# Performance work log

Measured on AMD Instinct MI355X. Metric: run time of the kernel, lower is better.

## Reference

```python
import itertools
import jax, jax.numpy as jnp
import numpy as np

FFT_LEN = 256      # kernel_size['ae']
HOP = 64           # frame hop
N_ANCHOR = 6
N_SPK = 2
NUM_STACKS = 4
N_DIL = 8          # dilations 1,2,...,128
EMBED = 20
OUTPUT_RATIO = 0.5
EPS = 1e-12        # tf.contrib.layers.layer_norm epsilon
DILS = [2 ** i for i in range(N_DIL)]
COMBS = np.array(list(itertools.combinations(range(N_ANCHOR), N_SPK)), np.int32)  # [15,2]
# sqrt of periodic hann window (scipy.signal.hann(256, sym=False))
WIN = np.sqrt(0.5 - 0.5 * np.cos(2.0 * np.pi * np.arange(FFT_LEN) / FFT_LEN)).astype(np.float32)
_wsq = WIN ** 2
_denom = np.tile(_wsq.reshape(FFT_LEN // HOP, HOP).sum(0), FFT_LEN // HOP)
INV_WIN = (WIN / _denom).astype(np.float32)  # tf.signal.inverse_stft_window_fn


def _prelu(x, a):
    return jnp.maximum(x, 0) + a * jnp.minimum(x, 0)


def _cln(x, g, b):  # layer norm over channel axis only (begin_norm_axis=2)
    m = x.mean(-1, keepdims=True)
    v = ((x - m) ** 2).mean(-1, keepdims=True)
    return (x - m) / jnp.sqrt(v + EPS) * g + b


def _gln(x, g, b):  # global layer norm over (time, channel) (begin_norm_axis=1)
    m = x.mean((1, 2), keepdims=True)
    v = ((x - m) ** 2).mean((1, 2), keepdims=True)
    return (x - m) / jnp.sqrt(v + EPS) * g + b


def _dwconv(x, w, di):  # x:[B,T,C], w:[K,C]; dilated depthwise conv, SAME padding
    C = x.shape[-1]
    return jax.lax.conv_general_dilated(
        x, w[:, None, :], (1,), 'SAME', rhs_dilation=(di,),
        dimension_numbers=('NWC', 'WIO', 'NWC'), feature_group_count=C)


def _ola(frames, hop):  # overlap-and-add: [.., T, K] -> [.., (T-1)*hop + K]
    lead = frames.shape[:-2]
    T, K = frames.shape[-2:]
    L = (T - 1) * hop + K
    idx = (np.arange(T)[:, None] * hop + np.arange(K)).reshape(-1)
    return jnp.zeros(lead + (L,), frames.dtype).at[..., idx].add(frames.reshape(lead + (T * K,)))


def _forward(audios, enc_w, enc_b, bottle_gamma, bottle_beta, bottle_w, bottle_b,
             blk_c1_w, blk_c1_b, blk_p1, blk_g1_g, blk_g1_b, blk_dw,
             blk_p2, blk_g2_g, blk_g2_b, blk_c2_w, blk_c2_b,
             sep_w, sep_b, anchors, dec_w, dec_b):
    B, _, L = audios.shape
    mix = audios.sum(1)                                   # [B,L]
    T = (L - FFT_LEN) // HOP + 1                          # 497 frames
    idx = np.arange(T)[:, None] * HOP + np.arange(FFT_LEN)
    frames = mix[:, idx]                                  # [B,T,256]
    enc = jax.nn.relu(jnp.einsum('btk,kf->btf', frames, enc_w) + enc_b)  # learned encoder
    spec = jnp.fft.rfft(frames * WIN)                     # STFT [B,T,129]
    mag = jnp.abs(spec)
    phase = jnp.arctan2(spec.imag, spec.real)
    x = _cln(jnp.concatenate([enc, jnp.log1p(mag)], -1), bottle_gamma, bottle_beta)
    x = x @ bottle_w + bottle_b                           # bottleneck 1x1 conv -> [B,T,256]
    for i in range(NUM_STACKS * N_DIL):                   # TCN dilated blocks
        di = DILS[i % N_DIL]
        y = x @ blk_c1_w[i] + blk_c1_b[i]
        y = _gln(_prelu(y, blk_p1[i]), blk_g1_g[i], blk_g1_b[i])
        y = _dwconv(y, blk_dw[i], di)
        y = _gln(_prelu(y, blk_p2[i]), blk_g2_g[i], blk_g2_b[i])
        x = x + (y @ blk_c2_w[i] + blk_c2_b[i])
    Fc = enc.shape[-1] + mag.shape[-1]                    # 385 = concat_channels
    emb = (x @ sep_w + sep_b).reshape(B, T, Fc, EMBED)    # [B,T,F,E]
    a_sets = anchors[COMBS]                               # [15,2,E]
    assign = jax.nn.softmax(jnp.einsum('btfe,pce->bptfc', emb, a_sets), axis=-1)
    attr = jnp.einsum('bptfc,btfe->bpce', assign, emb) / assign.sum((2, 3))[..., None]
    sp = jnp.einsum('bpce,bpde->bpcd', attr, attr)        # pairwise attractor similarity
    sp = jnp.where(jnp.eye(N_SPK, dtype=bool), -jnp.inf, sp)
    choice = jnp.argmin(sp.max((-1, -2)), axis=1)         # most dissimilar subset
    attractors = attr[jnp.arange(B), choice]              # [B,C,E]
    logits = jnp.einsum('btfe,bce->bctf', emb, attractors)
    feat = jnp.concatenate([enc, mag], -1)                # [B,T,F]
    code = logits * feat[:, None]                         # [B,C,T,F]
    ae_f = enc.shape[-1]
    conv_out = _ola(code[..., :ae_f] @ dec_w + dec_b, HOP)  # learned decoder branch
    ph = phase[:, None]
    sm = code[..., ae_f:]                                 # last stft_ch channels
    istft_frames = jnp.fft.irfft(jax.lax.complex(jnp.cos(ph) * sm, jnp.sin(ph) * sm), n=FFT_LEN)
    istft = _ola(istft_frames * INV_WIN, HOP)             # iSTFT branch
    return conv_out * OUTPUT_RATIO + istft * (1.0 - OUTPUT_RATIO)


def setup_inputs():
    B, S, L = 8, 2, 32000
    AE, BTL, H, K = 256, 256, 512, 3
    NB = NUM_STACKS * N_DIL
    FC = AE + FFT_LEN // 2 + 1
    ks = jax.random.split(jax.random.key(0), 9)
    rn = lambda k, sh, s=0.05: jax.random.normal(k, sh, jnp.float32) * s
    return {
        'audios': jax.random.normal(ks[0], (B, S, L), jnp.float32),
        'enc_w': rn(ks[1], (FFT_LEN, AE)),
        'enc_b': jnp.zeros((AE,), jnp.float32),
        'bottle_gamma': jnp.ones((FC,), jnp.float32),
        'bottle_beta': jnp.zeros((FC,), jnp.float32),
        'bottle_w': rn(ks[2], (FC, BTL)),
        'bottle_b': jnp.zeros((BTL,), jnp.float32),
        'blk_c1_w': rn(ks[3], (NB, BTL, H)),
        'blk_c1_b': jnp.zeros((NB, H), jnp.float32),
        'blk_p1': jnp.zeros((NB, H), jnp.float32),
        'blk_g1_g': jnp.ones((NB, H), jnp.float32),
        'blk_g1_b': jnp.zeros((NB, H), jnp.float32),
        'blk_dw': rn(ks[4], (NB, K, H), 0.2),
        'blk_p2': jnp.zeros((NB, H), jnp.float32),
        'blk_g2_g': jnp.ones((NB, H), jnp.float32),
        'blk_g2_b': jnp.zeros((NB, H), jnp.float32),
        'blk_c2_w': rn(ks[5], (NB, H, BTL)),
        'blk_c2_b': jnp.zeros((NB, BTL), jnp.float32),
        'sep_w': rn(ks[6], (BTL, FC * EMBED), 0.02),
        'sep_b': jnp.zeros((FC * EMBED,), jnp.float32),
        'anchors': rn(ks[7], (N_ANCHOR, EMBED), 0.1),
        'dec_w': rn(ks[8], (AE, FFT_LEN)),
        'dec_b': jnp.zeros((FFT_LEN,), jnp.float32),
    }


def reference(audios, enc_w, enc_b, bottle_gamma, bottle_beta, bottle_w, bottle_b,
              blk_c1_w, blk_c1_b, blk_p1, blk_g1_g, blk_g1_b, blk_dw,
              blk_p2, blk_g2_g, blk_g2_b, blk_c2_w, blk_c2_b,
              sep_w, sep_b, anchors, dec_w, dec_b):
    return _forward(audios, enc_w, enc_b, bottle_gamma, bottle_beta, bottle_w, bottle_b,
                    blk_c1_w, blk_c1_b, blk_p1, blk_g1_g, blk_g1_b, blk_dw,
                    blk_p2, blk_g2_g, blk_g2_b, blk_c2_w, blk_c2_b,
                    sep_w, sep_b, anchors, dec_w, dec_b)
```

## Files before the change

kernel.cpp:

```cpp
#include <hip/hip_runtime.h>
#include <math.h>

#define B_ 8
#define S_ 2
#define L_ 32000
#define T_ 497
#define AE 256
#define NFREQ 129
#define FC 385
#define XSTR 388
#define FRSTR 516
#define AFSTR 516
#define BTL 256
#define H_ 512
#define NB 32
#define EMBED 20
#define KB (T_*FC)
#define MEPS 1e-12f
#define PI2F 6.28318530717958647692f
#define MTOT (B_*T_)
#define SEPN 7700
#define SEPNT16 484
#define SEPBLK 7623

typedef __attribute__((ext_vector_type(8))) short bf16x8;
typedef __attribute__((ext_vector_type(4))) float f32x4;

__device__ __forceinline__ ushort f2bf(float f){
  union { float f; unsigned u; } x; x.f = f;
  unsigned r = x.u + 0x7FFFu + ((x.u >> 16) & 1u);
  return (ushort)(r >> 16);
}
__device__ __forceinline__ float bf2f(ushort h){
  union { unsigned u; float f; } x; x.u = ((unsigned)h) << 16;
  return x.f;
}

__device__ __forceinline__ float aldf(const float* p){
  return __hip_atomic_load(p, __ATOMIC_RELAXED, __HIP_MEMORY_SCOPE_AGENT);
}

static constexpr size_t ALGN(size_t x){ return (x + 63) & ~(size_t)63; }
static constexpr size_t o_bfr  = 0;
static constexpr size_t o_decB = ALGN(o_bfr + (size_t)256*516);
static constexpr size_t o_decBias = ALGN(o_decB + (size_t)514*256);
static constexpr size_t o_biasF  = ALGN(o_decBias + 256);
static constexpr size_t o_cf   = ALGN(o_biasF + 516);
static constexpr size_t o_mag  = ALGN(o_cf + (size_t)B_*T_*FRSTR);
static constexpr size_t o_cosp = ALGN(o_mag + (size_t)B_*T_*NFREQ);
static constexpr size_t o_sinp = ALGN(o_cosp + (size_t)B_*T_*NFREQ);
static constexpr size_t o_xln  = ALGN(o_sinp + (size_t)B_*T_*NFREQ);
static constexpr size_t o_x    = ALGN(o_xln + (size_t)B_*T_*XSTR);
static constexpr size_t o_y    = ALGN(o_x + (size_t)B_*T_*BTL);
static constexpr size_t o_z    = ALGN(o_y + (size_t)B_*T_*H_);
static constexpr size_t o_gsum = ALGN(o_z + (size_t)B_*T_*H_);
static constexpr size_t o_acc  = o_gsum + 1024;
static constexpr size_t o_att  = ALGN(o_acc + (size_t)B_*16*21);
static constexpr size_t o_emb  = ALGN(o_att + (size_t)B_*2*EMBED);
static constexpr size_t o_Af   = ALGN(o_emb + (size_t)B_*KB*EMBED);
static constexpr size_t o_w1p  = ALGN(o_Af + (size_t)2*B_*T_*AFSTR);
static constexpr size_t o_w2p  = ALGN(o_w1p + (size_t)2097152);
static constexpr size_t o_c1c2 = ALGN(o_w2p + (size_t)2097152);
static constexpr size_t o_bar  = ALGN(o_c1c2 + (size_t)32*512);
static constexpr size_t o_fr   = o_y;

#define PREP_BLOCKS 1034
#define PACKW_BLOCKS 32768
#define BIAS2_BLOCKS 256
#define PACKSEP_BLOCKS 7744

__global__ __launch_bounds__(256) void k_setup(
    const float* __restrict__ enc_w, const float* __restrict__ enc_b,
    const float* __restrict__ dec_w, const float* __restrict__ dec_b,
    const float* __restrict__ c1_w, const float* __restrict__ c2_w,
    const float* __restrict__ g2_g, const float* __restrict__ g2_b,
    const float* __restrict__ sep_w,
    float* __restrict__ bfr, float* __restrict__ decB,
    float* __restrict__ decBias, float* __restrict__ biasF,
    ushort* __restrict__ w1p, ushort* __restrict__ w2p,
    float* __restrict__ c1c2, ushort* __restrict__ w3p)
{
  int bx = blockIdx.x;
  if (bx < PREP_BLOCKS){
    int i = bx*256 + threadIdx.x;
    if (i < 256*516){
      int k = i / 516, n = i % 516;
      float v;
      if (n < 256) v = enc_w[(size_t)k*256 + n];
      else if (n < 514){
        int f2 = n - 256;
        float win = sqrtf(0.5f - 0.5f*cosf(PI2F * (float)k / 256.0f));
        int f = (f2 < NFREQ) ? f2 : (f2 - NFREQ);
        int m = (k * f) & 255;
        float th = PI2F * (float)m / 256.0f;
        v = (f2 < NFREQ) ? win * cosf(th) : -win * sinf(th);
      } else v = 0.f;
      bfr[i] = v;
      return;
    }
    int j = i - 256*516;
    if (j < 514*256){
      int k = j / 256, n = j & 255;
      float v;
      if (k < 256){
        v = 0.5f * dec_w[(size_t)k*256 + n];
      } else {
        int m = n & 63;
        float den = 0.f;
        #pragma unroll
        for (int q = 0; q < 4; q++) den += 0.5f - 0.5f*cosf(PI2F*(float)(m + 64*q)/256.0f);
        float win = sqrtf(0.5f - 0.5f*cosf(PI2F*(float)n/256.0f));
        float iw = win / den;
        int f = (k < 385) ? (k - 256) : (k - 385);
        int mm = (f * n) & 255;
        float th = PI2F * (float)mm / 256.0f;
        if (k < 385){
          float cf = (f==0 || f==128) ? 1.0f : 2.0f;
          v = 0.5f * iw * cf * cosf(th) * (1.0f/256.0f);
        } else {
          v = (f==0 || f==128) ? 0.0f : -1.0f * iw * sinf(th) * (1.0f/256.0f);
        }
      }
      decB[j] = v;
      return;
    }
    int jj = j - 514*256;
    if (jj < 256){ decBias[jj] = 0.5f * dec_b[jj]; return; }
    int n = jj - 256;
    if (n < 516) biasF[n] = (n < 256) ? enc_b[n] : 0.f;
    return;
  }
  if (bx < PREP_BLOCKS + PACKW_BLOCKS){
    size_t idx = (size_t)(bx - PREP_BLOCKS)*256 + threadIdx.x;
    const size_t PER = (size_t)32*131072;
    if (idx < PER){
      int i = (int)(idx >> 17);
      int o = (int)(idx & 131071);
      int kc = o >> 14;
      int n16 = (o >> 9) & 31;
      int l = (o >> 3) & 63;
      int j = o & 7;
      int k = kc*32 + (l>>4)*8 + j;
      int n = n16*16 + (l&15);
      w1p[idx] = f2bf(c1_w[((size_t)i*256 + k)*512 + n]);
    } else {
      size_t o2 = idx - PER;
      int i = (int)(o2 >> 17);
      int o = (int)(o2 & 131071);
      int kc = o >> 13;
      int n16 = (o >> 9) & 15;
      int l = (o >> 3) & 63;
      int j = o & 7;
      int k = kc*32 + (l>>4)*8 + j;
      int n = n16*16 + (l&15);
      w2p[o2] = f2bf(g2_g[(size_t)i*512 + k] * c2_w[((size_t)i*512 + k)*256 + n]);
    }
    return;
  }
  if (bx < PREP_BLOCKS + PACKW_BLOCKS + BIAS2_BLOCKS){
    int bi = bx - (PREP_BLOCKS + PACKW_BLOCKS);
    int i = bi >> 3, ks = bi & 7;
    int n = threadIdx.x;
    float s1 = 0.f, s2 = 0.f;
    for (int k = ks*64; k < ks*64 + 64; k++){
      float w = c2_w[((size_t)i*512 + k)*256 + n];
      s1 = fmaf(g2_b[(size_t)i*512 + k], w, s1);
      s2 = fmaf(g2_g[(size_t)i*512 + k], w, s2);
    }
    atomicAdd(&c1c2[(size_t)i*512 + n], s1);
    atomicAdd(&c1c2[(size_t)i*512 + 256 + n], s2);
    return;
  }
  {
    size_t idx = (size_t)(bx - (PREP_BLOCKS + PACKW_BLOCKS + BIAS2_BLOCKS))*256 + threadIdx.x;
    int j = (int)(idx & 7);
    int l = (int)((idx >> 3) & 63);
    int rest = (int)(idx >> 9);
    int n16 = rest % SEPNT16;
    int kc = rest / SEPNT16;
    int k = kc*32 + (l>>4)*8 + j;
    int n = n16*16 + (l&15);
    w3p[idx] = (n < SEPN) ? f2bf(sep_w[(size_t)k*SEPN + n]) : (ushort)0;
  }
}

template<int ALOAD>
__global__ __launch_bounds__(256, 2) void gemm3(
    const float* __restrict__ A, const float* __restrict__ Bm,
    const float* __restrict__ bias, float* __restrict__ C,
    int M, int N, int K, int lda, int ldb, int relu_cols)
{
  __shared__ float As[16][68];
  __shared__ float Bs[16][68];
  const int tid = threadIdx.x;
  const int tx = tid & 15, ty = tid >> 4;
  const int row0 = blockIdx.y*64, col0 = blockIdx.x*64;
  const int am = tid >> 2, ak = (tid & 3)*4;
  const int bk = tid >> 4, bn = (tid & 15)*4;
  const int arow = row0 + am;
  const bool aok = arow < M;
  const float* aptr = nullptr;
  const float* ap0 = nullptr; const float* ap1 = nullptr;
  if (ALOAD == 2){
    int r = aok ? arow : 0;
    int b = r / T_, t = r % T_;
    ap0 = A + ((size_t)b*2)*L_ + t*64;
    ap1 = ap0 + L_;
  } else {
    aptr = A + (size_t)(aok ? arow : 0)*lda;
  }
  const bool bfull = (col0 + 64 <= N);
  const int ksteps = (K+15) >> 4;

  float4 av, bv;

#define LOADA(ks_) { int k0 = (ks_) << 4; \
    av = make_float4(0.f,0.f,0.f,0.f); \
    if (aok){ \
      if (ALOAD == 2){ \
        float4 u = *(const float4*)(ap0 + k0 + ak); \
        float4 w = *(const float4*)(ap1 + k0 + ak); \
        av.x = u.x+w.x; av.y = u.y+w.y; av.z = u.z+w.z; av.w = u.w+w.w; \
      } else if (k0 + ak + 4 <= lda){ \
        av = *(const float4*)(aptr + k0 + ak); \
      } else { \
        float* pv = (float*)&av; \
        for (int j = 0; j < 4; j++){ int k = k0+ak+j; if (k < K) pv[j] = aptr[k]; } \
      } \
    } }

#define LOADB(ks_) { int k = ((ks_) << 4) + bk; \
    bv = make_float4(0.f,0.f,0.f,0.f); \
    if (k < K){ \
      if (bfull) bv = *(const float4*)(Bm + (size_t)k*ldb + col0 + bn); \
      else { float* pv = (float*)&bv; \
        for (int j = 0; j < 4; j++){ int c = col0+bn+j; if (c < N) pv[j] = Bm[(size_t)k*ldb + c]; } } } }

  float acc[4][4] = {};
  LOADA(0); LOADB(0);
  for (int ks = 0; ks < ksteps; ks++){
    As[ak+0][am] = av.x; As[ak+1][am] = av.y;
    As[ak+2][am] = av.z; As[ak+3][am] = av.w;
    *(float4*)&Bs[bk][bn] = bv;
    __syncthreads();
    if (ks + 1 < ksteps){ LOADA(ks+1); LOADB(ks+1); }
    #pragma unroll
    for (int kk = 0; kk < 16; kk++){
      float a4[4], b4[4];
      *(float4*)a4 = *(const float4*)&As[kk][ty*4];
      *(float4*)b4 = *(const float4*)&Bs[kk][tx*4];
      #pragma unroll
      for (int i = 0; i < 4; i++)
        #pragma unroll
        for (int j = 0; j < 4; j++) acc[i][j] = fmaf(a4[i], b4[j], acc[i][j]);
    }
    __syncthreads();
  }
#undef LOADA
#undef LOADB

  float bb4[4];
  #pragma unroll
  for (int j = 0; j < 4; j++){
    int c = col0 + tx*4 + j;
    bb4[j] = (bias && c < N) ? bias[c] : 0.f;
  }
  #pragma unroll
  for (int i = 0; i < 4; i++){
    int r_l = row0 + ty*4 + i;
    if (r_l >= M) continue;
    size_t r_g = (size_t)r_l;
    int c0 = col0 + tx*4;
    if (bfull){
      float4 o; float* po = (float*)&o;
      #pragma unroll
      for (int j = 0; j < 4; j++){
        float v = acc[i][j] + bb4[j];
        if (c0 + j < relu_cols) v = fmaxf(v, 0.f);
        po[j] = v;
      }
      *(float4*)(C + r_g*N + c0) = o;
    } else {
      #pragma unroll
      for (int j = 0; j < 4; j++){
        int c = c0 + j;
        if (c >= N) continue;
        float v = acc[i][j] + bb4[j];
        if (c < relu_cols) v = fmaxf(v, 0.f);
        C[r_g*N + c] = v;
      }
    }
  }
}

__global__ __launch_bounds__(256, 2) void k_sep(
    const ushort* __restrict__ xb, const ushort* __restrict__ wp,
    const float* __restrict__ bias, float* __restrict__ C)
{
  int id = blockIdx.x;
  int xcd = id & 7, sub = id >> 3;
  const int q = SEPBLK/8, r = SEPBLK%8;
  int lin = (xcd < r ? xcd*(q+1) : r*(q+1) + (xcd - r)*q) + sub;
  int nb = lin/63, mt = lin%63;
  int tid = threadIdx.x;
  int wv = tid >> 6, l = tid & 63;
  int row0 = mt*64 + wv*16;
  int lm = l & 15, lq = l >> 4;
  int row = row0 + lm;
  int rclamp = (row < MTOT) ? row : (MTOT-1);
  int n0 = nb*64;
  const ushort* ap = xb + (size_t)rclamp*256;
  f32x4 acc[4] = {};
  #pragma unroll
  for (int kc = 0; kc < 8; kc++){
    bf16x8 a = *(const bf16x8*)(ap + kc*32 + lq*8);
    #pragma unroll
    for (int nt = 0; nt < 4; nt++){
      bf16x8 bfv = *(const bf16x8*)(wp + (((size_t)kc*SEPNT16 + (n0>>4) + nt)*64 + l)*8);
      acc[nt] = __builtin_amdgcn_mfma_f32_16x16x32_bf16(a, bfv, acc[nt], 0, 0, 0);
    }
  }
  #pragma unroll
  for (int nt = 0; nt < 4; nt++){
    int col = n0 + nt*16 + lm;
    if (col >= SEPN) continue;
    float bb = bias[col];
    #pragma unroll
    for (int r2 = 0; r2 < 4; r2++){
      int t = row0 + lq*4 + r2;
      if (t < MTOT) C[(size_t)t*SEPN + col] = acc[nt][r2] + bb;
    }
  }
}

__device__ __forceinline__ void pbar(unsigned* bar, int grp){
  __syncthreads();
  if (threadIdx.x == 0){
    unsigned* g = bar + grp*64;
    unsigned gen = __hip_atomic_load(g+32, __ATOMIC_RELAXED, __HIP_MEMORY_SCOPE_AGENT);
    unsigned p = gen & 1u;
    unsigned a = __hip_atomic_fetch_add(g+p, 1u, __ATOMIC_RELAXED, __HIP_MEMORY_SCOPE_AGENT);
    if (a == 63u){
      __hip_atomic_store(g+p, 0u, __ATOMIC_RELAXED, __HIP_MEMORY_SCOPE_AGENT);
      __hip_atomic_store(g+32, gen+1u, __ATOMIC_RELAXED, __HIP_MEMORY_SCOPE_AGENT);
    } else {
      while (__hip_atomic_load(g+32, __ATOMIC_RELAXED, __HIP_MEMORY_SCOPE_AGENT) == gen)
        __builtin_amdgcn_s_sleep(1);
    }
    asm volatile("buffer_inv sc0" ::: "memory");
  }
  __syncthreads();
}

__global__ __launch_bounds__(256, 2) void k_tcn(
    float* __restrict__ x0, float* __restrict__ x1,
    float* __restrict__ Ubuf, ushort* __restrict__ yb,
    const ushort* __restrict__ w1pA, const ushort* __restrict__ w2pA,
    const float* __restrict__ c1bA, const float* __restrict__ p1A,
    const float* __restrict__ g1gA, const float* __restrict__ g1bA,
    const float* __restrict__ dwA, const float* __restrict__ p2A,
    const float* __restrict__ c2bA, const float* __restrict__ ccA,
    float* __restrict__ gsum, unsigned* bar)
{
  __shared__ float red[8];
  __shared__ float cst[3072];
  const int tid = threadIdx.x;
  const int wv = tid >> 6, l = tid & 63;
  const int bid = blockIdx.x;
  const int b = bid & 7, mt = (bid >> 3) & 7, nb = bid >> 6;
  const int row0 = mt*64 + wv*16;
  const int lm = l & 15, lq = l >> 4;
  const int row = row0 + lm;
  const bool rok = row < T_;
  const size_t rbase = ((size_t)b*T_ + row)*256;
  const float icnt = 1.f/((float)T_*(float)H_);

  for (int i = 0; i < NB; i++){
    {
      const float* xr = (i == 0) ? x0 : (((i-1)&1) ? x1 : x0);
      float* xw = (i & 1) ? x1 : x0;
      const ushort* w1p = w1pA + (size_t)i*131072;
      const float* bias = c1bA + (size_t)i*H_;
      const float* pa   = p1A + (size_t)i*H_;
      float* gs = gsum + i*32;
      const int hasU = (i > 0) ? 1 : 0;
      const float* c2bPrev = c2bA + (size_t)((i > 0) ? (i-1) : 0)*BTL;
      const float* ccPrev  = ccA  + (size_t)((i > 0) ? (i-1) : 0)*512;
      const float* gsPrev  = (i == 0) ? gsum : (gsum + (i-1)*32 + 16);

      float rstd2 = 0.f;
      if (hasU){
        float m2 = aldf(gsPrev + b*2)*icnt;
        rstd2 = rsqrtf(aldf(gsPrev + b*2 + 1)*icnt - m2*m2 + MEPS);
        float mr = m2*rstd2;
        cst[tid] = c2bPrev[tid] + ccPrev[tid] - mr*ccPrev[256 + tid];
      }
      __syncthreads();
      int n0 = nb*64;
      f32x4 acc[4] = {};
      #pragma unroll 4
      for (int kc = 0; kc < 8; kc++){
        int k0 = kc*32 + lq*8;
        float xv[8];
        *(float4*)&xv[0] = *(const float4*)(xr + rbase + k0);
        *(float4*)&xv[4] = *(const float4*)(xr + rbase + k0 + 4);
        if (hasU){
          float uv[8], av8[8];
          *(float4*)&uv[0]  = *(const float4*)(Ubuf + rbase + k0);
          *(float4*)&uv[4]  = *(const float4*)(Ubuf + rbase + k0 + 4);
          *(float4*)&av8[0] = *(float4*)&cst[k0];
          *(float4*)&av8[4] = *(float4*)&cst[k0 + 4];
          #pragma unroll
          for (int j = 0; j < 8; j++)
            xv[j] = xv[j] + rstd2*uv[j] + av8[j];
          if (nb == 0 && rok){
            *(float4*)(xw + rbase + k0)     = *(float4*)&xv[0];
            *(float4*)(xw + rbase + k0 + 4) = *(float4*)&xv[4];
          }
        }
        bf16x8 a;
        #pragma unroll
        for (int j = 0; j < 8; j++) a[j] = (short)f2bf(xv[j]);
        #pragma unroll
        for (int nt = 0; nt < 4; nt++){
          bf16x8 bf = __builtin_nontemporal_load(
              (const bf16x8*)(w1p + (((size_t)kc*32 + (n0>>4) + nt)*64 + l)*8));
          acc[nt] = __builtin_amdgcn_mfma_f32_16x16x32_bf16(a, bf, acc[nt], 0, 0, 0);
        }
      }
      float ps = 0.f, pss = 0.f;
      #pragma unroll
      for (int nt = 0; nt < 4; nt++){
        int col = n0 + nt*16 + lm;
        float bb = bias[col], pav = pa[col];
        #pragma unroll
        for (int r = 0; r < 4; r++){
          int t = row0 + lq*4 + r;
          if (t < T_){
            float v = acc[nt][r] + bb;
            float p = fmaxf(v, 0.f) + pav*fminf(v, 0.f);
            yb[((size_t)b*T_ + t)*512 + col] = f2bf(p);
            ps += p; pss += p*p;
          }
        }
      }
      #pragma unroll
      for (int off = 32; off > 0; off >>= 1){
        ps  += __shfl_down(ps, off);
        pss += __shfl_down(pss, off);
      }
      if (l == 0){ red[wv*2] = ps; red[wv*2+1] = pss; }
      __syncthreads();
      if (tid == 0) atomicAdd(&gs[b*2],   red[0]+red[2]+red[4]+red[6]);
      if (tid == 1) atomicAdd(&gs[b*2+1], red[1]+red[3]+red[5]+red[7]);
    }
    pbar(bar, b);
    {
      const int dil = 1 << (i & 7);
      const ushort* w2p = w2pA + (size_t)i*131072;
      const float* dwk = dwA + (size_t)i*3*H_;
      const float* gg  = g1gA + (size_t)i*H_;
      const float* gb  = g1bA + (size_t)i*H_;
      const float* pa  = p2A + (size_t)i*H_;
      const float* gs1 = gsum + i*32;
      float* gs2 = gsum + i*32 + 16;

      float m1 = aldf(gs1 + b*2)*icnt;
      float rstd1 = rsqrtf(aldf(gs1 + b*2 + 1)*icnt - m1*m1 + MEPS);
      #pragma unroll
      for (int qq = 0; qq < 2; qq++){
        int c = tid + qq*256;
        float ga_ = gg[c]*rstd1;
        cst[c]        = ga_;
        cst[512 + c]  = gb[c] - m1*ga_;
        cst[1024 + c] = dwk[c];
        cst[1536 + c] = dwk[H_ + c];
        cst[2048 + c] = dwk[2*H_ + c];
        cst[2560 + c] = pa[c];
      }
      __syncthreads();
      int n0 = nb*32;
      f32x4 acc[2] = {};
      float sp = 0.f, spp = 0.f;
      const bool dostat = (nb == 0) && rok;
      #pragma unroll 4
      for (int kc = 0; kc < 16; kc++){
        int ch0 = kc*32 + lq*8;
        float ga8[8], ba8[8];
        *(float4*)&ga8[0] = *(float4*)&cst[ch0];
        *(float4*)&ga8[4] = *(float4*)&cst[ch0 + 4];
        *(float4*)&ba8[0] = *(float4*)&cst[512 + ch0];
        *(float4*)&ba8[4] = *(float4*)&cst[512 + ch0 + 4];
        float z[8] = {0.f,0.f,0.f,0.f,0.f,0.f,0.f,0.f};
        #pragma unroll
        for (int kk = 0; kk < 3; kk++){
          int tt = row + (kk-1)*dil;
          if (tt >= 0 && tt < T_){
            bf16x8 yv = *(const bf16x8*)(yb + ((size_t)b*T_ + tt)*512 + ch0);
            float d8[8];
            *(float4*)&d8[0] = *(float4*)&cst[1024 + kk*512 + ch0];
            *(float4*)&d8[4] = *(float4*)&cst[1024 + kk*512 + ch0 + 4];
            #pragma unroll
            for (int j = 0; j < 8; j++)
              z[j] = fmaf(d8[j], bf2f((ushort)yv[j])*ga8[j] + ba8[j], z[j]);
          }
        }
        float pa8[8];
        *(float4*)&pa8[0] = *(float4*)&cst[2560 + ch0];
        *(float4*)&pa8[4] = *(float4*)&cst[2560 + ch0 + 4];
        bf16x8 a;
        #pragma unroll
        for (int j = 0; j < 8; j++){
          float p = fmaxf(z[j], 0.f) + pa8[j]*fminf(z[j], 0.f);
          if (dostat){ sp += p; spp += p*p; }
          a[j] = (short)f2bf(p);
        }
        #pragma unroll
        for (int nt = 0; nt < 2; nt++){
          bf16x8 bf = __builtin_nontemporal_load(
              (const bf16x8*)(w2p + (((size_t)kc*16 + (n0>>4) + nt)*64 + l)*8));
          acc[nt] = __builtin_amdgcn_mfma_f32_16x16x32_bf16(a, bf, acc[nt], 0, 0, 0);
        }
      }
      #pragma unroll
      for (int nt = 0; nt < 2; nt++){
        int col = n0 + nt*16 + lm;
        #pragma unroll
        for (int r = 0; r < 4; r++){
          int tr = row0 + lq*4 + r;
          if (tr < T_) Ubuf[((size_t)b*T_ + tr)*256 + col] = acc[nt][r];
        }
      }
      if (nb == 0){
        #pragma unroll
        for (int off = 32; off > 0; off >>= 1){
          sp  += __shfl_down(sp, off);
          spp += __shfl_down(spp, off);
        }
        if (l == 0){ red[wv*2] = sp; red[wv*2+1] = spp; }
        __syncthreads();
        if (tid == 0) atomicAdd(&gs2[b*2],   red[0]+red[2]+red[4]+red[6]);
        if (tid == 1) atomicAdd(&gs2[b*2+1], red[1]+red[3]+red[5]+red[7]);
      }
    }
    if (i < NB-1) pbar(bar, b);
  }
}

__global__ __launch_bounds__(256) void k_applyx(
    const float* __restrict__ xr, const float* __restrict__ U,
    const float* __restrict__ gs, const float* __restrict__ c2b,
    const float* __restrict__ cc, ushort* __restrict__ xo)
{
  int i = blockIdx.x*256 + threadIdx.x;
  if (i < B_*T_*256){
    int b = i / (T_*256);
    int k = i & 255;
    const float icnt = 1.f/((float)T_*(float)H_);
    float m = gs[b*2]*icnt;
    float rstd = rsqrtf(gs[b*2+1]*icnt - m*m + MEPS);
    float mr = m*rstd;
    xo[i] = f2bf(xr[i] + rstd*U[i] + c2b[k] + cc[k] - mr*cc[256 + k]);
  }
}

__global__ __launch_bounds__(256) void k_cln(
    const float* __restrict__ cf,
    const float* __restrict__ gamma, const float* __restrict__ beta,
    float* __restrict__ mag, float* __restrict__ cosp, float* __restrict__ sinp,
    float* __restrict__ xln){
  int t = blockIdx.x, b = blockIdx.y, tid = threadIdx.x;
  size_t row = (size_t)b*T_ + t;
  __shared__ float feat[FC];
  __shared__ float red[8];
  feat[tid] = cf[row*FRSTR + tid];
  if (tid < NFREQ){
    float re = cf[row*FRSTR + 256 + tid], im = cf[row*FRSTR + 385 + tid];
    float m = sqrtf(re*re + im*im);
    mag[row*NFREQ + tid] = m;
    float c = 1.f, s = 0.f;
    if (m > 0.f){ c = re/m; s = im/m; }
    cosp[row*NFREQ + tid] = c;
    sinp[row*NFREQ + tid] = s;
    feat[AE + tid] = log1pf(m);
  }
  __syncthreads();
  float v = feat[tid] + ((tid < FC-256) ? feat[256+tid] : 0.f);
  #pragma unroll
  for (int off = 32; off > 0; off >>= 1) v += __shfl_down(v, off);
  if ((tid & 63) == 0) red[tid>>6] = v;
  __syncthreads();
  float mean = (red[0]+red[1]+red[2]+red[3]) * (1.0f/FC);
  float d0 = feat[tid] - mean;
  float vv = d0*d0;
  if (tid < FC-256){ float d1 = feat[256+tid] - mean; vv += d1*d1; }
  __syncthreads();
  #pragma unroll
  for (int off = 32; off > 0; off >>= 1) vv += __shfl_down(vv, off);
  if ((tid & 63) == 0) red[tid>>6] = vv;
  __syncthreads();
  float var = (red[0]+red[1]+red[2]+red[3]) * (1.0f/FC);
  float rstd = rsqrtf(var + MEPS);
  xln[row*XSTR + tid] = (feat[tid]-mean)*rstd*gamma[tid] + beta[tid];
  if (tid < FC-256)
    xln[row*XSTR + 256+tid] = (feat[256+tid]-mean)*rstd*gamma[256+tid] + beta[256+tid];
  if (tid < XSTR-FC) xln[row*XSTR + FC + tid] = 0.f;
}

#define ATTR_CH 16
__global__ __launch_bounds__(256) void k_attr2(const float* __restrict__ emb,
                                               const float* __restrict__ anchors,
                                               float* __restrict__ acc){
  const int c0a[16] = {0,0,0,0,0,1,1,1,1,2,2,2,3,3,4,0};
  const int c1a[16] = {1,2,3,4,5,2,3,4,5,3,4,5,4,5,5,0};
  int by = blockIdx.y;
  int b = by >> 2, g = by & 3;
  int tid = threadIdx.x;
  __shared__ float anc[6][20];
  __shared__ float wred[4][84];
  if (tid < 120) anc[tid/20][tid%20] = anchors[tid];
  __syncthreads();
  float ar[4][21];
  #pragma unroll
  for (int q = 0; q < 4; q++)
    #pragma unroll
    for (int e = 0; e < 21; e++) ar[q][e] = 0.f;
  const float* eb = emb + (size_t)b*KB*EMBED;
  for (int k = blockIdx.x*256 + tid; k < KB; k += ATTR_CH*256){
    float e[20];
    const float4* p = (const float4*)(eb + (size_t)k*EMBED);
    #pragma unroll
    for (int i = 0; i < 5; i++){
      float4 v = p[i];
      e[4*i] = v.x; e[4*i+1] = v.y; e[4*i+2] = v.z; e[4*i+3] = v.w;
    }
    float d[6];
    #pragma unroll
    for (int c = 0; c < 6; c++){
      float s = 0.f;
      #pragma unroll
      for (int j = 0; j < 20; j++) s = fmaf(e[j], anc[c][j], s);
      d[c] = s;
    }
    #pragma unroll
    for (int q = 0; q < 4; q++){
      int s = g*4 + q;
      float w = (s == 15) ? 1.0f : 1.0f / (1.0f + expf(d[c1a[s]] - d[c0a[s]]));
      #pragma unroll
      for (int j = 0; j < 20; j++) ar[q][j] = fmaf(w, e[j], ar[q][j]);
      ar[q][20] += w;
    }
  }
  #pragma unroll
  for (int q = 0; q < 4; q++)
    #pragma unroll
    for (int e = 0; e < 21; e++)
      #pragma unroll
      for (int off = 32; off > 0; off >>= 1)
        ar[q][e] += __shfl_down(ar[q][e], off);
  if ((tid & 63) == 0){
    int w = tid >> 6;
    #pragma unroll
    for (int q = 0; q < 4; q++)
      #pragma unroll
      for (int e = 0; e < 21; e++) wred[w][q*21+e] = ar[q][e];
  }
  __syncthreads();
  if (tid < 84){
    float s = wred[0][tid] + wred[1][tid] + wred[2][tid] + wred[3][tid];
    int q = tid / 21, e = tid % 21;
    atomicAdd(&acc[((size_t)b*16 + g*4 + q)*21 + e], s);
  }
}

__global__ __launch_bounds__(128) void k_attrfin2(const float* __restrict__ acc,
                                                  float* __restrict__ attractors){
  __shared__ float aN[120][40];
  __shared__ float sp[120];
  int tid = threadIdx.x;
  if (tid < 120){
    int b = tid / 15, p = tid % 15;
    const float* ap = acc + ((size_t)b*16 + p)*21;
    const float* ae = acc + ((size_t)b*16 + 15)*21;
    float den0 = ap[20];
    float den1 = (float)KB - den0;
    float s = 0.f;
    for (int e = 0; e < 20; e++){
      float a0 = ap[e] / den0;
      float a1 = (ae[e] - ap[e]) / den1;
      aN[tid][e] = a0; aN[tid][20+e] = a1;
      s = fmaf(a0, a1, s);
    }
    sp[tid] = s;
  }
  __syncthreads();
  if (tid < B_){
    int base = tid * 15, best = 0;
    float bv = sp[base];
    for (int p = 1; p < 15; p++) if (sp[base+p] < bv){ bv = sp[base+p]; best = p; }
    for (int i = 0; i < 40; i++) attractors[tid*40 + i] = aN[base+best][i];
  }
}

__global__ __launch_bounds__(256) void k_afull(
    const float* __restrict__ emb, const float* __restrict__ cf,
    const float* __restrict__ mag, const float* __restrict__ cosp,
    const float* __restrict__ sinp, const float* __restrict__ attractors,
    float* __restrict__ Af){
  int t = blockIdx.x, b = blockIdx.y, tid = threadIdx.x;
  __shared__ float att[40];
  if (tid < 40) att[tid] = attractors[b*40 + tid];
  __syncthreads();
  size_t row = (size_t)b*T_ + t;
  size_t r0 = ((size_t)(b*2+0)*T_ + t)*AFSTR;
  size_t r1 = ((size_t)(b*2+1)*T_ + t)*AFSTR;
  for (int f = tid; f < FC; f += 256){
    const float* e = emb + (row*FC + f)*20;
    float l0 = 0.f, l1 = 0.f;
    #pragma unroll
    for (int j = 0; j < 20; j++){
      float ev = e[j];
      l0 = fmaf(ev, att[j],    l0);
      l1 = fmaf(ev, att[20+j], l1);
    }
    if (f < AE){
      float ft = cf[row*FRSTR + f];
      Af[r0 + f] = l0*ft;
      Af[r1 + f] = l1*ft;
    } else {
      int fi = f - AE;
      float ft = mag[row*NFREQ + fi];
      float c = cosp[row*NFREQ + fi], s = sinp[row*NFREQ + fi];
      float s0 = l0*ft, s1v = l1*ft;
      Af[r0 + 256 + fi] = c*s0;  Af[r0 + 385 + fi] = s*s0;
      Af[r1 + 256 + fi] = c*s1v; Af[r1 + 385 + fi] = s*s1v;
    }
  }
  if (tid < 2){
    Af[r0 + 514 + tid] = 0.f;
    Af[r1 + 514 + tid] = 0.f;
  }
}

__global__ __launch_bounds__(256) void k_ola(const float* __restrict__ frames,
                                             float* __restrict__ out){
  int i = blockIdx.x*256 + threadIdx.x;
  if (i < B_*2*L_){
    int bs = i / L_, l = i % L_;
    int t0 = l >> 6;
    float s = 0.f;
    #pragma unroll
    for (int j = 0; j < 4; j++){
      int t = t0 - j;
      if (t >= 0 && t < T_){
        int k = l - t*64;
        s += frames[((size_t)bs*T_ + t)*256 + k];
      }
    }
    out[i] = s;
  }
}

extern "C" void kernel_launch(void* const* d_in, const int* in_sizes, int n_in,
                              void* d_out, int out_size, void* d_ws, size_t ws_size,
                              hipStream_t stream) {
  const float* audios   = (const float*)d_in[0];
  const float* enc_w    = (const float*)d_in[1];
  const float* enc_b    = (const float*)d_in[2];
  const float* bgamma   = (const float*)d_in[3];
  const float* bbeta    = (const float*)d_in[4];
  const float* bottle_w = (const float*)d_in[5];
  const float* bottle_b = (const float*)d_in[6];
  const float* c1_w     = (const float*)d_in[7];
  const float* c1_b     = (const float*)d_in[8];
  const float* p1       = (const float*)d_in[9];
  const float* g1_g     = (const float*)d_in[10];
  const float* g1_b     = (const float*)d_in[11];
  const float* dwp      = (const float*)d_in[12];
  const float* p2       = (const float*)d_in[13];
  const float* g2_g     = (const float*)d_in[14];
  const float* g2_b     = (const float*)d_in[15];
  const float* c2_w     = (const float*)d_in[16];
  const float* c2_b     = (const float*)d_in[17];
  const float* sep_w    = (const float*)d_in[18];
  const float* sep_b    = (const float*)d_in[19];
  const float* anchors  = (const float*)d_in[20];
  const float* dec_w    = (const float*)d_in[21];
  const float* dec_b    = (const float*)d_in[22];

  float* ws = (float*)d_ws;
  float* bfr   = ws + o_bfr;
  float* decB  = ws + o_decB;
  float* decBias = ws + o_decBias;
  float* biasF = ws + o_biasF;
  float* cf    = ws + o_cf;
  float* mag   = ws + o_mag;
  float* cosp  = ws + o_cosp;
  float* sinp  = ws + o_sinp;
  float* xln   = ws + o_xln;
  float* xbuf0 = ws + o_x;
  float* xbuf1 = ws + o_y;
  float* Ubuf  = ws + o_y + (size_t)B_*T_*BTL;
  float* gsum  = ws + o_gsum;
  float* accp  = ws + o_acc;
  float* attp  = ws + o_att;
  float* embp  = ws + o_emb;
  float* Afull = ws + o_Af;
  float* framesp = ws + o_fr;
  float* c1c2  = ws + o_c1c2;
  unsigned* barp = (unsigned*)(ws + o_bar);
  ushort* w1p  = (ushort*)(ws + o_w1p);
  ushort* w2p  = (ushort*)(ws + o_w2p);
  ushort* w3p  = (ushort*)(ws + o_Af);
  ushort* xb16 = (ushort*)(ws + o_xln);
  ushort* yb16 = (ushort*)(ws + o_z);

  hipMemsetAsync((void*)gsum, 0, (1024 + (size_t)B_*16*21) * sizeof(float), stream);
  hipMemsetAsync((void*)c1c2, 0, (size_t)32*512*sizeof(float), stream);
  hipMemsetAsync((void*)barp, 0, 1024*sizeof(float), stream);

  k_setup<<<PREP_BLOCKS + PACKW_BLOCKS + BIAS2_BLOCKS + PACKSEP_BLOCKS, 256, 0, stream>>>(
      enc_w, enc_b, dec_w, dec_b, c1_w, c2_w, g2_g, g2_b, sep_w,
      bfr, decB, decBias, biasF, w1p, w2p, c1c2, w3p);

  gemm3<2><<<dim3(9, 63), 256, 0, stream>>>(
      audios, bfr, biasF, cf, B_*T_, FRSTR, 256, 0, FRSTR, 256);

  k_cln<<<dim3(T_, B_), 256, 0, stream>>>(cf, bgamma, bbeta, mag, cosp, sinp, xln);

  gemm3<0><<<dim3(4, 63), 256, 0, stream>>>(
      xln, bottle_w, bottle_b, xbuf0, B_*T_, BTL, FC, XSTR, BTL, 0);

  k_tcn<<<dim3(512), dim3(256), 0, stream>>>(
      xbuf0, xbuf1, Ubuf, yb16, w1p, w2p,
      c1_b, p1, g1_g, g1_b, dwp, p2, c2_b, c1c2, gsum, barp);

  k_applyx<<<(B_*T_*256 + 255)/256, 256, 0, stream>>>(
      xbuf1, Ubuf, gsum + (NB-1)*32 + 16,
      c2_b + (size_t)(NB-1)*BTL, c1c2 + (size_t)(NB-1)*512, xb16);

  k_sep<<<dim3(SEPBLK), 256, 0, stream>>>(xb16, w3p, sep_b, embp);

  k_attr2<<<dim3(ATTR_CH, B_*4), 256, 0, stream>>>(embp, anchors, accp);
  k_attrfin2<<<1, 128, 0, stream>>>(accp, attp);

  k_afull<<<dim3(T_, B_), 256, 0, stream>>>(embp, cf, mag, cosp, sinp, attp, Afull);
  gemm3<0><<<dim3(4, 125), 256, 0, stream>>>(
      Afull, decB, decBias, framesp, 2*B_*T_, 256, 514, AFSTR, BTL, 0);
  k_ola<<<(B_*2*L_ + 255)/256, 256, 0, stream>>>(framesp, (float*)d_out);
}
```

Before: 1.748 ms.

## Split TCN block K-loops across two wave groups with LDS reduction

Doubles the persistent TCN block to 512 threads and splits the K dimension of both per-block GEMMs between two halves of the waves. The upper half writes its partial MFMA accumulators to shared memory and the lower half adds them before the epilogue. This shortens each wave's serial K chain and raises wave count per CU to hide load latency. In exchange it adds an extra __syncthreads, LDS traffic, and a larger shared footprint per block.

Measured after the change: 2.577 ms. 47.4% more time.

```diff
diff --git a/kernel.cpp b/kernel.cpp
--- a/kernel.cpp
+++ b/kernel.cpp
@@ -352,7 +352,7 @@
   __syncthreads();
 }
 
-__global__ __launch_bounds__(256, 2) void k_tcn(
+__global__ __launch_bounds__(512, 4) void k_tcn(
     float* __restrict__ x0, float* __restrict__ x1,
     float* __restrict__ Ubuf, ushort* __restrict__ yb,
     const ushort* __restrict__ w1pA, const ushort* __restrict__ w2pA,
@@ -362,13 +362,15 @@
     const float* __restrict__ c2bA, const float* __restrict__ ccA,
     float* __restrict__ gsum, unsigned* bar)
 {
-  __shared__ float red[8];
+  __shared__ float red[16];
   __shared__ float cst[3072];
+  __shared__ float swp[4096];
   const int tid = threadIdx.x;
   const int wv = tid >> 6, l = tid & 63;
+  const int rowgrp = wv & 3, kchalf = wv >> 2;
   const int bid = blockIdx.x;
   const int b = bid & 7, mt = (bid >> 3) & 7, nb = bid >> 6;
-  const int row0 = mt*64 + wv*16;
+  const int row0 = mt*64 + rowgrp*16;
   const int lm = l & 15, lq = l >> 4;
   const int row = row0 + lm;
   const bool rok = row < T_;
@@ -393,13 +395,14 @@
         float m2 = aldf(gsPrev + b*2)*icnt;
         rstd2 = rsqrtf(aldf(gsPrev + b*2 + 1)*icnt - m2*m2 + MEPS);
         float mr = m2*rstd2;
-        cst[tid] = c2bPrev[tid] + ccPrev[tid] - mr*ccPrev[256 + tid];
+        if (tid < 256) cst[tid] = c2bPrev[tid] + ccPrev[tid] - mr*ccPrev[256 + tid];
       }
       __syncthreads();
       int n0 = nb*64;
       f32x4 acc[4] = {};
-      #pragma unroll 4
-      for (int kc = 0; kc < 8; kc++){
+      #pragma unroll
+      for (int kci = 0; kci < 4; kci++){
+        int kc = kchalf*4 + kci;
         int k0 = kc*32 + lq*8;
         float xv[8];
         *(float4*)&xv[0] = *(const float4*)(xr + rbase + k0);
@@ -428,19 +431,33 @@
           acc[nt] = __builtin_amdgcn_mfma_f32_16x16x32_bf16(a, bf, acc[nt], 0, 0, 0);
         }
       }
+      if (kchalf == 1){
+        #pragma unroll
+        for (int nt = 0; nt < 4; nt++)
+          *(f32x4*)&swp[(((size_t)rowgrp*64 + l)*4 + nt)*4] = acc[nt];
+      }
+      __syncthreads();
       float ps = 0.f, pss = 0.f;
-      #pragma unroll
-      for (int nt = 0; nt < 4; nt++){
-        int col = n0 + nt*16 + lm;
-        float bb = bias[col], pav = pa[col];
-        #pragma unroll
-        for (int r = 0; r < 4; r++){
-          int t = row0 + lq*4 + r;
-          if (t < T_){
-            float v = acc[nt][r] + bb;
-            float p = fmaxf(v, 0.f) + pav*fminf(v, 0.f);
-            yb[((size_t)b*T_ + t)*512 + col] = f2bf(p);
-            ps += p; pss += p*p;
+      if (kchalf == 0){
+        #pragma unroll
+        for (int nt = 0; nt < 4; nt++){
+          f32x4 o = *(f32x4*)&swp[(((size_t)rowgrp*64 + l)*4 + nt)*4];
+          acc[nt][0] += o[0]; acc[nt][1] += o[1];
+          acc[nt][2] += o[2]; acc[nt][3] += o[3];
+        }
+        #pragma unroll
+        for (int nt = 0; nt < 4; nt++){
+          int col = n0 + nt*16 + lm;
+          float bb = bias[col], pav = pa[col];
+          #pragma unroll
+          for (int r = 0; r < 4; r++){
+            int t = row0 + lq*4 + r;
+            if (t < T_){
+              float v = acc[nt][r] + bb;
+              float p = fmaxf(v, 0.f) + pav*fminf(v, 0.f);
+              yb[((size_t)b*T_ + t)*512 + col] = f2bf(p);
+              ps += p; pss += p*p;
+            }
           }
         }
       }
@@ -449,7 +466,7 @@
         ps  += __shfl_down(ps, off);
         pss += __shfl_down(pss, off);
       }
-      if (l == 0){ red[wv*2] = ps; red[wv*2+1] = pss; }
+      if (l == 0 && kchalf == 0){ red[rowgrp*2] = ps; red[rowgrp*2+1] = pss; }
       __syncthreads();
       if (tid == 0) atomicAdd(&gs[b*2],   red[0]+red[2]+red[4]+red[6]);
       if (tid == 1) atomicAdd(&gs[b*2+1], red[1]+red[3]+red[5]+red[7]);
@@ -467,9 +484,8 @@
 
       float m1 = aldf(gs1 + b*2)*icnt;
       float rstd1 = rsqrtf(aldf(gs1 + b*2 + 1)*icnt - m1*m1 + MEPS);
-      #pragma unroll
-      for (int qq = 0; qq < 2; qq++){
-        int c = tid + qq*256;
+      {
+        int c = tid;
         float ga_ = gg[c]*rstd1;
         cst[c]        = ga_;
         cst[512 + c]  = gb[c] - m1*ga_;
@@ -483,8 +499,9 @@
       f32x4 acc[2] = {};
       float sp = 0.f, spp = 0.f;
       const bool dostat = (nb == 0) && rok;
-      #pragma unroll 4
-      for (int kc = 0; kc < 16; kc++){
+      #pragma unroll
+      for (int kci = 0; kci < 8; kci++){
+        int kc = kchalf*8 + kci;
         int ch0 = kc*32 + lq*8;
         float ga8[8], ba8[8];
         *(float4*)&ga8[0] = *(float4*)&cst[ch0];
@@ -522,13 +539,27 @@
           acc[nt] = __builtin_amdgcn_mfma_f32_16x16x32_bf16(a, bf, acc[nt], 0, 0, 0);
         }
       }
-      #pragma unroll
-      for (int nt = 0; nt < 2; nt++){
-        int col = n0 + nt*16 + lm;
-        #pragma unroll
-        for (int r = 0; r < 4; r++){
-          int tr = row0 + lq*4 + r;
-          if (tr < T_) Ubuf[((size_t)b*T_ + tr)*256 + col] = acc[nt][r];
+      if (kchalf == 1){
+        #pragma unroll
+        for (int nt = 0; nt < 2; nt++)
+          *(f32x4*)&swp[(((size_t)rowgrp*64 + l)*2 + nt)*4] = acc[nt];
+      }
+      __syncthreads();
+      if (kchalf == 0){
+        #pragma unroll
+        for (int nt = 0; nt < 2; nt++){
+          f32x4 o = *(f32x4*)&swp[(((size_t)rowgrp*64 + l)*2 + nt)*4];
+          acc[nt][0] += o[0]; acc[nt][1] += o[1];
+          acc[nt][2] += o[2]; acc[nt][3] += o[3];
+        }
+        #pragma unroll
+        for (int nt = 0; nt < 2; nt++){
+          int col = n0 + nt*16 + lm;
+          #pragma unroll
+          for (int r = 0; r < 4; r++){
+            int tr = row0 + lq*4 + r;
+            if (tr < T_) Ubuf[((size_t)b*T_ + tr)*256 + col] = acc[nt][r];
+          }
         }
       }
       if (nb == 0){
@@ -539,8 +570,10 @@
         }
         if (l == 0){ red[wv*2] = sp; red[wv*2+1] = spp; }
         __syncthreads();
-        if (tid == 0) atomicAdd(&gs2[b*2],   red[0]+red[2]+red[4]+red[6]);
-        if (tid == 1) atomicAdd(&gs2[b*2+1], red[1]+red[3]+red[5]+red[7]);
+        if (tid == 0) atomicAdd(&gs2[b*2],
+          red[0]+red[2]+red[4]+red[6]+red[8]+red[10]+red[12]+red[14]);
+        if (tid == 1) atomicAdd(&gs2[b*2+1],
+          red[1]+red[3]+red[5]+red[7]+red[9]+red[11]+red[13]+red[15]);
       }
     }
     if (i < NB-1) pbar(bar, b);
@@ -831,7 +864,7 @@
   gemm3<0><<<dim3(4, 63), 256, 0, stream>>>(
       xln, bottle_w, bottle_b, xbuf0, B_*T_, BTL, FC, XSTR, BTL, 0);
 
-  k_tcn<<<dim3(512), dim3(256), 0, stream>>>(
+  k_tcn<<<dim3(512), dim3(512), 0, stream>>>(
       xbuf0, xbuf1, Ubuf, yb16, w1p, w2p,
       c1_b, p1, g1_g, g1_b, dwp, p2, c2_b, c1c2, gsum, barp);
 
```
